# Performance work log

Measured on AMD Instinct MI355X. Metric: run time of the kernel, lower is better.

## Reference

```python
import jax, jax.numpy as jnp
import numpy as np
from jax import lax

B, C, H, W = 32, 3, 256, 256
P, D, E, K = 16, 256, 8, 2
HP, WP = H // P, W // P
N = HP * WP
GATE_IN = C * P * P  # 768
GATE_HID = D // 2    # 128


def _mk(key, shape, scale=0.02):
    return scale * jax.random.normal(key, shape, dtype=jnp.float32)


def setup_inputs() -> dict:
    key = jax.random.key(0)
    ks = jax.random.split(key, 20)
    inp = {
        "x": jax.random.normal(ks[0], (B, C, H, W), dtype=jnp.float32),
        # gate MLP: Linear(768,128) -> ReLU -> Linear(128,8)
        "g_w1": _mk(ks[1], (GATE_HID, GATE_IN)),
        "g_b1": jnp.zeros((GATE_HID,), jnp.float32),
        "g_w2": _mk(ks[2], (E, GATE_HID)),
        "g_b2": jnp.zeros((E,), jnp.float32),
        # per-expert CNN params, stacked with leading expert dim E
        "dw1_w": _mk(ks[3], (E, 3, 1, 3, 3)),   "dw1_b": jnp.zeros((E, 3), jnp.float32),
        "pw1_w": _mk(ks[4], (E, 64, 3, 1, 1)),  "pw1_b": jnp.zeros((E, 64), jnp.float32),
        "dw2_w": _mk(ks[5], (E, 64, 1, 3, 3)),  "dw2_b": jnp.zeros((E, 64), jnp.float32),
        "pw2_w": _mk(ks[6], (E, 128, 64, 1, 1)), "pw2_b": jnp.zeros((E, 128), jnp.float32),
        "dw3_w": _mk(ks[7], (E, 128, 1, 3, 3)), "dw3_b": jnp.zeros((E, 128), jnp.float32),
        "pw3_w": _mk(ks[8], (E, D, 128, 1, 1)), "pw3_b": jnp.zeros((E, D), jnp.float32),
    }
    return inp


def _dwconv(x, w, b, stride):
    # depthwise 3x3, padding 1; x: [n, c, h, w]; w: [c, 1, 3, 3]
    c = x.shape[1]
    y = lax.conv_general_dilated(
        x, w, (stride, stride), ((1, 1), (1, 1)),
        dimension_numbers=("NCHW", "OIHW", "NCHW"), feature_group_count=c)
    return jax.nn.relu(y + b[None, :, None, None])


def _pwconv(x, w, b):
    # pointwise 1x1 conv as GEMM; w: [o, c, 1, 1]
    y = jnp.einsum("nchw,oc->nohw", x, w[:, :, 0, 0]) + b[None, :, None, None]
    return jax.nn.relu(y)


def _expert(x, dw1w, dw1b, pw1w, pw1b, dw2w, dw2b, pw2w, pw2b, dw3w, dw3b, pw3w, pw3b):
    # x: [BN, 3, 16, 16] -> [BN, D]
    x = _pwconv(_dwconv(x, dw1w, dw1b, 2), pw1w, pw1b)   # [BN, 64, 8, 8]
    x = _pwconv(_dwconv(x, dw2w, dw2b, 2), pw2w, pw2b)   # [BN, 128, 4, 4]
    x = _pwconv(_dwconv(x, dw3w, dw3b, 2), pw3w, pw3b)   # [BN, 256, 2, 2]
    return x.mean(axis=(2, 3))                            # adaptive avg pool to 1x1


def reference(x, g_w1, g_b1, g_w2, g_b2,
              dw1_w, dw1_b, pw1_w, pw1_b, dw2_w, dw2_b, pw2_w, pw2_b,
              dw3_w, dw3_b, pw3_w, pw3_b):
    b = x.shape[0]
    # nn.Unfold(kernel=P, stride=P): columns ordered (c, di, dj)
    patches = x.reshape(b, C, HP, P, WP, P).transpose(0, 2, 4, 1, 3, 5)  # [B,hp,wp,C,P,P]
    patches_sp = patches.reshape(b * N, C, P, P)
    patches_flat = patches_sp.reshape(b * N, GATE_IN)

    # gate (eval mode: dropout is identity)
    h = jax.nn.relu(patches_flat @ g_w1.T + g_b1)
    logits = h @ g_w2.T + g_b2                       # [BN, E]
    topk_vals, topk_idx = lax.top_k(logits, K)       # [BN, K]
    weights = jax.nn.softmax(topk_vals, axis=-1)
    one_hot = jax.nn.one_hot(topk_idx, E, dtype=x.dtype)   # [BN, K, E]
    routing = (one_hot * weights[..., None]).sum(axis=1)   # [BN, E]

    # run all experts densely (as the original does), then combine
    expert_outs = jax.vmap(_expert, in_axes=(None,) + (0,) * 12)(
        patches_sp, dw1_w, dw1_b, pw1_w, pw1_b, dw2_w, dw2_b,
        pw2_w, pw2_b, dw3_w, dw3_b, pw3_w, pw3_b)   # [E, BN, D]
    out = jnp.einsum("ne,end->nd", routing, expert_outs)  # [BN, D]

    features = out.reshape(b, HP, WP, D).transpose(0, 3, 1, 2)  # [B, D, hp, wp]
    load_balance_loss = jnp.float32(0.0)  # eval mode
    return features, load_balance_loss
```

## Files before the change

kernel.cpp:

```cpp
#include <hip/hip_runtime.h>

#define BN 8192
#define GIN 768
#define SL 2560

#define O_ROUTE_I 0UL
#define O_ROUTE_W (O_ROUTE_I + (size_t)BN*2*4)
#define O_COUNTS  (O_ROUTE_W + (size_t)BN*2*4)
#define O_LISTS   (O_COUNTS + 256)
#define O_PW2T    (O_LISTS + (size_t)8*BN*4)
#define O_PW3T    (O_PW2T + (size_t)8*64*128*4)
#define O_SLOT    (O_PW3T + (size_t)8*128*256*4)

__global__ __launch_bounds__(256) void k0_prep(const float* __restrict__ pw2w,
                                               const float* __restrict__ pw3w,
                                               float* __restrict__ pw2t,
                                               float* __restrict__ pw3t,
                                               int* __restrict__ counts)
{
    int tid = blockIdx.x * 256 + threadIdx.x;
    if (tid < 8) counts[tid] = 0;
    for (int idx = tid; idx < 8 * 128 * 64; idx += 256 * 256) {
        int e = idx >> 13; int r = idx & 8191; int oc = r >> 6; int c = r & 63;
        pw2t[(size_t)e * 8192 + c * 128 + oc] = pw2w[idx];
    }
    for (int idx = tid; idx < 8 * 256 * 128; idx += 256 * 256) {
        int e = idx >> 15; int r = idx & 32767; int oc = r >> 7; int c = r & 127;
        pw3t[(size_t)e * 32768 + c * 256 + oc] = pw3w[idx];
    }
}

__global__ __launch_bounds__(256) void k1_gate(
    const float* __restrict__ x, const float* __restrict__ w1,
    const float* __restrict__ b1, const float* __restrict__ w2,
    const float* __restrict__ b2,
    int* __restrict__ route_i, float* __restrict__ route_w,
    int* __restrict__ counts, int* __restrict__ lists)
{
    __shared__ __align__(16) float A[32][20];
    __shared__ __align__(16) float Wl[32][132];
    __shared__ float hl[16][132];
    __shared__ float ll[16][8];

    int tid = threadIdx.x;
    int pblk = blockIdx.x * 16;

    int pgrp = tid & 7;
    int hgrp = tid >> 3;
    float acc[2][4] = {};

    int sp  = tid >> 4;
    int sk2 = (tid & 15) * 2;
    int swh = tid >> 1;
    int swk = (tid & 1) * 16;

    int patchA = pblk + sp;
    int bA = patchA >> 8; int nA = patchA & 255; int hpA = nA >> 4; int wpA = nA & 15;

    for (int kc = 0; kc < GIN; kc += 32) {
        {
            int k = kc + sk2;
            int c = k >> 8; int rem = k & 255; int ri = rem >> 4; int j = rem & 15;
            const float* src = x + (((size_t)(bA * 3 + c) * 256 + hpA * 16 + ri) * 256 + wpA * 16 + j);
            float2 a2 = *reinterpret_cast<const float2*>(src);
            A[sk2][sp] = a2.x; A[sk2 + 1][sp] = a2.y;
        }
        {
            const float* wsrc = w1 + (size_t)swh * GIN + kc + swk;
            #pragma unroll
            for (int qq = 0; qq < 4; qq++) {
                float4 w4 = *reinterpret_cast<const float4*>(wsrc + qq * 4);
                Wl[swk + qq * 4 + 0][swh] = w4.x; Wl[swk + qq * 4 + 1][swh] = w4.y;
                Wl[swk + qq * 4 + 2][swh] = w4.z; Wl[swk + qq * 4 + 3][swh] = w4.w;
            }
        }
        __syncthreads();
        float cacc[2][4] = {};
        #pragma unroll
        for (int k2 = 0; k2 < 32; k2++) {
            float2 av = *reinterpret_cast<const float2*>(&A[k2][pgrp * 2]);
            float4 wv = *reinterpret_cast<const float4*>(&Wl[k2][hgrp * 4]);
            float aa[2] = {av.x, av.y};
            float ww[4] = {wv.x, wv.y, wv.z, wv.w};
            #pragma unroll
            for (int i = 0; i < 2; i++) {
                #pragma unroll
                for (int jj = 0; jj < 4; jj++) cacc[i][jj] += aa[i] * ww[jj];
            }
        }
        #pragma unroll
        for (int i = 0; i < 2; i++) {
            #pragma unroll
            for (int jj = 0; jj < 4; jj++) acc[i][jj] += cacc[i][jj];
        }
        __syncthreads();
    }

    #pragma unroll
    for (int jj = 0; jj < 4; jj++) {
        float bb = b1[hgrp * 4 + jj];
        #pragma unroll
        for (int i = 0; i < 2; i++) {
            float v = acc[i][jj] + bb;
            hl[pgrp * 2 + i][hgrp * 4 + jj] = v > 0.f ? v : 0.f;
        }
    }
    __syncthreads();

    if (tid < 128) {
        int lp = tid >> 3; int le = tid & 7;
        float lacc = b2[le];
        const float* wrow = w2 + le * 128;
        for (int h = 0; h < 128; h++) lacc += hl[lp][h] * wrow[h];
        ll[lp][le] = lacc;
    }
    __syncthreads();

    if (tid < 16) {
        int patch = pblk + tid;
        float v[8];
        #pragma unroll
        for (int e = 0; e < 8; e++) v[e] = ll[tid][e];
        int e0 = 0; float m0 = v[0];
        #pragma unroll
        for (int e = 1; e < 8; e++) if (v[e] > m0) { m0 = v[e]; e0 = e; }
        int e1 = -1; float m1 = -3.0e38f;
        #pragma unroll
        for (int e = 0; e < 8; e++) if (e != e0 && v[e] > m1) { m1 = v[e]; e1 = e; }
        float t = expf(m1 - m0);
        float w0 = 1.f / (1.f + t);
        float w1v = t * w0;
        route_i[patch * 2] = e0; route_i[patch * 2 + 1] = e1;
        route_w[patch * 2] = w0; route_w[patch * 2 + 1] = w1v;
        int p0 = atomicAdd(&counts[e0], 1);
        lists[e0 * BN + p0] = patch * 2;
        int p1 = atomicAdd(&counts[e1], 1);
        lists[e1 * BN + p1] = patch * 2 + 1;
    }
}

__global__ __launch_bounds__(256, 4) void k23_expert(
    const float* __restrict__ x, const int* __restrict__ counts,
    const int* __restrict__ lists,
    const float* __restrict__ dw1w, const float* __restrict__ dw1b,
    const float* __restrict__ pw1w, const float* __restrict__ pw1b,
    const float* __restrict__ dw2w, const float* __restrict__ dw2b,
    const float* __restrict__ pw2t, const float* __restrict__ pw2b,
    const float* __restrict__ dw3w, const float* __restrict__ dw3b,
    const float* __restrict__ pw3t, const float* __restrict__ pw3b,
    float* __restrict__ slot)
{
    __shared__ __align__(16) float buf[4][SL];

    int e = blockIdx.x & 7;
    int chunk = blockIdx.x >> 3;
    int cnt = counts[e];
    int base = chunk * 4;
    if (base >= cnt) return;
    int n_en = cnt - base; if (n_en > 4) n_en = 4;
    int tid = threadIdx.x;
    int wid = tid >> 6;
    int l = tid & 63;
    int en_l = l >> 4;
    int q = l & 15;

    int myidx = base + wid; if (myidx >= cnt) myidx = cnt - 1;
    int pslot = lists[e * BN + myidx];
    int patch = pslot >> 1;
    int b = patch >> 8, nn = patch & 255, hp = nn >> 4, wp = nn & 15;

    float* pl  = buf[wid];
    float* d1  = buf[wid] + 2048;
    float* d2t = buf[wid];

    {
        int r = l >> 2; int j4 = (l & 3) * 4;
        #pragma unroll
        for (int c = 0; c < 3; c++) {
            const float* src = x + (((size_t)(b * 3 + c) * 256 + hp * 16 + r) * 256 + wp * 16 + j4);
            float4 v = *reinterpret_cast<const float4*>(src);
            *reinterpret_cast<float4*>(&pl[c * 320 + r * 20 + j4]) = v;
        }
    }

    {
        int oh = l >> 3, ow = l & 7;
        #pragma unroll
        for (int c = 0; c < 3; c++) {
            const float* w9 = dw1w + (e * 3 + c) * 9;
            float acc = dw1b[e * 3 + c];
            #pragma unroll
            for (int ki = 0; ki < 3; ki++) {
                int ih = oh * 2 - 1 + ki;
                if ((unsigned)ih < 16u) {
                    #pragma unroll
                    for (int kj = 0; kj < 3; kj++) {
                        int iw = ow * 2 - 1 + kj;
                        if ((unsigned)iw < 16u) acc += pl[c * 320 + ih * 20 + iw] * w9[ki * 3 + kj];
                    }
                }
            }
            d1[c * 64 + l] = acc > 0.f ? acc : 0.f;
        }
    }

    {
        const float* w3 = pw1w + (e * 64 + l) * 3;
        float pw0 = w3[0], pw1v = w3[1], pw2v = w3[2];
        float pb = pw1b[e * 64 + l];
        const float* w9 = dw2w + (e * 64 + l) * 9;
        float wd[9];
        #pragma unroll
        for (int i = 0; i < 9; i++) wd[i] = w9[i];
        float bd = dw2b[e * 64 + l];

        int dcol = (l + wid * 4) & 63;
        float rc[8] = {};
        float re[8], ro[8];

        #pragma unroll
        for (int oh = 0; oh < 4; oh++) {
            #pragma unroll
            for (int half = 0; half < 2; half++) {
                float* dst = half ? ro : re;
                const float* d1b = d1 + (oh * 2 + half) * 8;
                float4 x0 = *reinterpret_cast<const float4*>(&d1b[0]);
                float4 x1 = *reinterpret_cast<const float4*>(&d1b[4]);
                float4 y0 = *reinterpret_cast<const float4*>(&d1b[64]);
                float4 y1 = *reinterpret_cast<const float4*>(&d1b[68]);
                float4 z0 = *reinterpret_cast<const float4*>(&d1b[128]);
                float4 z1 = *reinterpret_cast<const float4*>(&d1b[132]);
                float v;
                v = pb + x0.x * pw0 + y0.x * pw1v + z0.x * pw2v; dst[0] = v > 0.f ? v : 0.f;
                v = pb + x0.y * pw0 + y0.y * pw1v + z0.y * pw2v; dst[1] = v > 0.f ? v : 0.f;
                v = pb + x0.z * pw0 + y0.z * pw1v + z0.z * pw2v; dst[2] = v > 0.f ? v : 0.f;
                v = pb + x0.w * pw0 + y0.w * pw1v + z0.w * pw2v; dst[3] = v > 0.f ? v : 0.f;
                v = pb + x1.x * pw0 + y1.x * pw1v + z1.x * pw2v; dst[4] = v > 0.f ? v : 0.f;
                v = pb + x1.y * pw0 + y1.y * pw1v + z1.y * pw2v; dst[5] = v > 0.f ? v : 0.f;
                v = pb + x1.z * pw0 + y1.z * pw1v + z1.z * pw2v; dst[6] = v > 0.f ? v : 0.f;
                v = pb + x1.w * pw0 + y1.w * pw1v + z1.w * pw2v; dst[7] = v > 0.f ? v : 0.f;
            }
            #pragma unroll
            for (int ow = 0; ow < 4; ow++) {
                float acc = bd;
                if (oh > 0) {
                    #pragma unroll
                    for (int kj = 0; kj < 3; kj++) {
                        int iw = ow * 2 - 1 + kj;
                        if ((unsigned)iw < 8u) acc += rc[iw] * wd[kj];
                    }
                }
                #pragma unroll
                for (int kj = 0; kj < 3; kj++) {
                    int iw = ow * 2 - 1 + kj;
                    if ((unsigned)iw < 8u) acc += re[iw] * wd[3 + kj];
                }
                #pragma unroll
                for (int kj = 0; kj < 3; kj++) {
                    int iw = ow * 2 - 1 + kj;
                    if ((unsigned)iw < 8u) acc += ro[iw] * wd[6 + kj];
                }
                d2t[(oh * 4 + ow) * 68 + dcol] = acc > 0.f ? acc : 0.f;
            }
            #pragma unroll
            for (int i = 0; i < 8; i++) rc[i] = ro[i];
        }
    }
    __syncthreads();

    {
        const float* dsl = buf[en_l];
        int ocg = q & 3, pq = q >> 2;
        int oc0 = wid * 32 + ocg * 8;
        int p0 = pq * 4;
        float acc[8][4] = {};
        const float* wbase = pw2t + (size_t)e * 8192;
        #pragma unroll 2
        for (int c4 = 0; c4 < 16; c4++) {
            int col = (c4 * 4 + en_l * 4) & 63;
            float4 a0 = *reinterpret_cast<const float4*>(&dsl[(p0 + 0) * 68 + col]);
            float4 a1 = *reinterpret_cast<const float4*>(&dsl[(p0 + 1) * 68 + col]);
            float4 a2 = *reinterpret_cast<const float4*>(&dsl[(p0 + 2) * 68 + col]);
            float4 a3 = *reinterpret_cast<const float4*>(&dsl[(p0 + 3) * 68 + col]);
            float av[4][4] = {{a0.x, a1.x, a2.x, a3.x}, {a0.y, a1.y, a2.y, a3.y},
                              {a0.z, a1.z, a2.z, a3.z}, {a0.w, a1.w, a2.w, a3.w}};
            #pragma unroll
            for (int cc = 0; cc < 4; cc++) {
                int c = c4 * 4 + cc;
                float4 wa = *reinterpret_cast<const float4*>(wbase + c * 128 + oc0);
                float4 wb = *reinterpret_cast<const float4*>(wbase + c * 128 + oc0 + 4);
                float wv[8] = {wa.x, wa.y, wa.z, wa.w, wb.x, wb.y, wb.z, wb.w};
                #pragma unroll
                for (int j = 0; j < 8; j++) {
                    #pragma unroll
                    for (int i = 0; i < 4; i++) acc[j][i] += wv[j] * av[cc][i];
                }
            }
        }
        __syncthreads();
        int g = oc0 >> 3;
        float* p2w = buf[en_l];
        #pragma unroll
        for (int j = 0; j < 8; j++) {
            float bb = pw2b[e * 128 + oc0 + j];
            #pragma unroll
            for (int i = 0; i < 4; i++) {
                float v = acc[j][i] + bb;
                p2w[(oc0 + j) * 16 + ((p0 + i + g + en_l) & 15)] = v > 0.f ? v : 0.f;
            }
        }
    }
    __syncthreads();

    {
        float* p2 = buf[wid];
        float* d3 = buf[wid] + 2048;
        #pragma unroll
        for (int chb = 0; chb < 128; chb += 64) {
            int ch = chb + l;
            int grp = ch >> 3;
            const float* w9 = dw3w + (e * 128 + ch) * 9;
            float bb = dw3b[e * 128 + ch];
            #pragma unroll
            for (int pos = 0; pos < 4; pos++) {
                int oh = pos >> 1, ow = pos & 1;
                float acc = bb;
                #pragma unroll
                for (int ki = 0; ki < 3; ki++) {
                    int ih = oh * 2 - 1 + ki;
                    if ((unsigned)ih < 4u) {
                        #pragma unroll
                        for (int kj = 0; kj < 3; kj++) {
                            int iw = ow * 2 - 1 + kj;
                            if ((unsigned)iw < 4u)
                                acc += p2[ch * 16 + ((ih * 4 + iw + grp + wid) & 15)] * w9[ki * 3 + kj];
                        }
                    }
                }
                d3[((ch + wid * 4) & 127) * 4 + pos] = acc > 0.f ? acc : 0.f;
            }
        }
    }
    __syncthreads();

    {
        int oc0 = wid * 64 + q * 4;
        const float* d3b = buf[en_l] + 2048;
        const float* wbase = pw3t + (size_t)e * 32768;
        float acc[4][4] = {};
        #pragma unroll 4
        for (int c = 0; c < 128; c++) {
            float4 a = *reinterpret_cast<const float4*>(&d3b[((c + en_l * 4) & 127) * 4]);
            float4 w = *reinterpret_cast<const float4*>(wbase + c * 256 + oc0);
            float av[4] = {a.x, a.y, a.z, a.w};
            float wv[4] = {w.x, w.y, w.z, w.w};
            #pragma unroll
            for (int j = 0; j < 4; j++) {
                #pragma unroll
                for (int i = 0; i < 4; i++) acc[j][i] += wv[j] * av[i];
            }
        }
        if (en_l < n_en) {
            int ps_f = lists[e * BN + base + en_l];
            float o4[4];
            #pragma unroll
            for (int j = 0; j < 4; j++) {
                float bb = pw3b[e * 256 + oc0 + j];
                float s = 0.f;
                #pragma unroll
                for (int i = 0; i < 4; i++) {
                    float v = acc[j][i] + bb;
                    s += (v > 0.f ? v : 0.f);
                }
                o4[j] = 0.25f * s;
            }
            *reinterpret_cast<float4*>(slot + (size_t)ps_f * 256 + oc0) =
                make_float4(o4[0], o4[1], o4[2], o4[3]);
        }
    }
}

__global__ __launch_bounds__(256) void k4_comb(
    const float* __restrict__ slot, const float* __restrict__ route_w,
    float* __restrict__ out)
{
    __shared__ float cl[16][257];
    int bx = blockIdx.x;
    int b = bx >> 4; int hp = bx & 15;
    int tid = threadIdx.x;
    int d = tid;
    for (int wp = 0; wp < 16; wp++) {
        int n = (b * 16 + hp) * 16 + wp;
        float w0 = route_w[n * 2], w1 = route_w[n * 2 + 1];
        float v = w0 * slot[(size_t)(n * 2) * 256 + d] + w1 * slot[(size_t)(n * 2 + 1) * 256 + d];
        cl[wp][d] = v;
    }
    __syncthreads();
    int wp = tid & 15; int dg = tid >> 4;
    for (int r = 0; r < 16; r++) {
        int dd = r * 16 + dg;
        out[(((size_t)b * 256 + dd) * 16 + hp) * 16 + wp] = cl[wp][dd];
    }
    if (bx == 0 && tid == 0) out[(size_t)BN * 256] = 0.0f;
}

extern "C" void kernel_launch(void* const* d_in, const int* in_sizes, int n_in,
                              void* d_out, int out_size, void* d_ws, size_t ws_size,
                              hipStream_t stream)
{
    const float* x    = (const float*)d_in[0];
    const float* gw1  = (const float*)d_in[1];
    const float* gb1  = (const float*)d_in[2];
    const float* gw2  = (const float*)d_in[3];
    const float* gb2  = (const float*)d_in[4];
    const float* dw1w = (const float*)d_in[5];
    const float* dw1b = (const float*)d_in[6];
    const float* pw1w = (const float*)d_in[7];
    const float* pw1b = (const float*)d_in[8];
    const float* dw2w = (const float*)d_in[9];
    const float* dw2b = (const float*)d_in[10];
    const float* pw2w = (const float*)d_in[11];
    const float* pw2b = (const float*)d_in[12];
    const float* dw3w = (const float*)d_in[13];
    const float* dw3b = (const float*)d_in[14];
    const float* pw3w = (const float*)d_in[15];
    const float* pw3b = (const float*)d_in[16];

    char* ws = (char*)d_ws;
    int*   route_i = (int*)(ws + O_ROUTE_I);
    float* route_w = (float*)(ws + O_ROUTE_W);
    int*   counts  = (int*)(ws + O_COUNTS);
    int*   lists   = (int*)(ws + O_LISTS);
    float* pw2t    = (float*)(ws + O_PW2T);
    float* pw3t    = (float*)(ws + O_PW3T);
    float* slot    = (float*)(ws + O_SLOT);
    float* out     = (float*)d_out;

    hipLaunchKernelGGL(k0_prep, dim3(256), dim3(256), 0, stream,
                       pw2w, pw3w, pw2t, pw3t, counts);
    hipLaunchKernelGGL(k1_gate, dim3(BN / 16), dim3(256), 0, stream,
                       x, gw1, gb1, gw2, gb2, route_i, route_w, counts, lists);
    hipLaunchKernelGGL(k23_expert, dim3(8 * 2048), dim3(256), 0, stream,
                       x, counts, lists, dw1w, dw1b, pw1w, pw1b, dw2w, dw2b,
                       pw2t, pw2b, dw3w, dw3b, pw3t, pw3b, slot);
    hipLaunchKernelGGL(k4_comb, dim3(512), dim3(256), 0, stream,
                       slot, route_w, out);
}
```

Before: 520.2 us.

## Double expert kernel block to 512 threads, splitting each patch's stages across two waves

The expert kernel now launches 512 threads per block, with two wavefronts per patch instead of one. The dw2 rows, the dw3 channels and the pw2/pw3 output channels are split between the two waves, which halves per-thread accumulators and work. A new barrier is added after the dw1 stage, and that stage is done by only half the waves. The aim is more parallelism and latency hiding per block at the cost of extra synchronisation, some duplicated pw1 row computation, and idle waves during dw1.

```diff
diff --git a/kernel.cpp b/kernel.cpp
--- a/kernel.cpp
+++ b/kernel.cpp
@@ -139,7 +139,58 @@
     }
 }
 
-__global__ __launch_bounds__(256, 4) void k23_expert(
+__device__ __forceinline__ void pw1_row(const float* __restrict__ d1, int row,
+                                        float pb, float pw0, float pw1v, float pw2v,
+                                        float* __restrict__ dst)
+{
+    const float* d1b = d1 + row * 8;
+    float4 x0 = *reinterpret_cast<const float4*>(&d1b[0]);
+    float4 x1 = *reinterpret_cast<const float4*>(&d1b[4]);
+    float4 y0 = *reinterpret_cast<const float4*>(&d1b[64]);
+    float4 y1 = *reinterpret_cast<const float4*>(&d1b[68]);
+    float4 z0 = *reinterpret_cast<const float4*>(&d1b[128]);
+    float4 z1 = *reinterpret_cast<const float4*>(&d1b[132]);
+    float v;
+    v = pb + x0.x * pw0 + y0.x * pw1v + z0.x * pw2v; dst[0] = v > 0.f ? v : 0.f;
+    v = pb + x0.y * pw0 + y0.y * pw1v + z0.y * pw2v; dst[1] = v > 0.f ? v : 0.f;
+    v = pb + x0.z * pw0 + y0.z * pw1v + z0.z * pw2v; dst[2] = v > 0.f ? v : 0.f;
+    v = pb + x0.w * pw0 + y0.w * pw1v + z0.w * pw2v; dst[3] = v > 0.f ? v : 0.f;
+    v = pb + x1.x * pw0 + y1.x * pw1v + z1.x * pw2v; dst[4] = v > 0.f ? v : 0.f;
+    v = pb + x1.y * pw0 + y1.y * pw1v + z1.y * pw2v; dst[5] = v > 0.f ? v : 0.f;
+    v = pb + x1.z * pw0 + y1.z * pw1v + z1.z * pw2v; dst[6] = v > 0.f ? v : 0.f;
+    v = pb + x1.w * pw0 + y1.w * pw1v + z1.w * pw2v; dst[7] = v > 0.f ? v : 0.f;
+}
+
+__device__ __forceinline__ void dw2_row(int oh, bool use_rc,
+                                        const float* rc, const float* re, const float* ro,
+                                        const float* wd, float bd,
+                                        float* __restrict__ d2t, int dcol)
+{
+    #pragma unroll
+    for (int ow = 0; ow < 4; ow++) {
+        float acc = bd;
+        if (use_rc) {
+            #pragma unroll
+            for (int kj = 0; kj < 3; kj++) {
+                int iw = ow * 2 - 1 + kj;
+                if ((unsigned)iw < 8u) acc += rc[iw] * wd[kj];
+            }
+        }
+        #pragma unroll
+        for (int kj = 0; kj < 3; kj++) {
+            int iw = ow * 2 - 1 + kj;
+            if ((unsigned)iw < 8u) acc += re[iw] * wd[3 + kj];
+        }
+        #pragma unroll
+        for (int kj = 0; kj < 3; kj++) {
+            int iw = ow * 2 - 1 + kj;
+            if ((unsigned)iw < 8u) acc += ro[iw] * wd[6 + kj];
+        }
+        d2t[(oh * 4 + ow) * 68 + dcol] = acc > 0.f ? acc : 0.f;
+    }
+}
+
+__global__ __launch_bounds__(512, 8) void k23_expert(
     const float* __restrict__ x, const int* __restrict__ counts,
     const int* __restrict__ lists,
     const float* __restrict__ dw1w, const float* __restrict__ dw1b,
@@ -161,48 +212,52 @@
     int tid = threadIdx.x;
     int wid = tid >> 6;
     int l = tid & 63;
+    int en_p = wid & 3;
+    int half = wid >> 2;
     int en_l = l >> 4;
     int q = l & 15;
 
-    int myidx = base + wid; if (myidx >= cnt) myidx = cnt - 1;
+    int myidx = base + en_p; if (myidx >= cnt) myidx = cnt - 1;
     int pslot = lists[e * BN + myidx];
     int patch = pslot >> 1;
     int b = patch >> 8, nn = patch & 255, hp = nn >> 4, wp = nn & 15;
 
-    float* pl  = buf[wid];
-    float* d1  = buf[wid] + 2048;
-    float* d2t = buf[wid];
-
-    {
-        int r = l >> 2; int j4 = (l & 3) * 4;
-        #pragma unroll
-        for (int c = 0; c < 3; c++) {
-            const float* src = x + (((size_t)(b * 3 + c) * 256 + hp * 16 + r) * 256 + wp * 16 + j4);
-            float4 v = *reinterpret_cast<const float4*>(src);
-            *reinterpret_cast<float4*>(&pl[c * 320 + r * 20 + j4]) = v;
-        }
-    }
-
-    {
-        int oh = l >> 3, ow = l & 7;
-        #pragma unroll
-        for (int c = 0; c < 3; c++) {
-            const float* w9 = dw1w + (e * 3 + c) * 9;
-            float acc = dw1b[e * 3 + c];
-            #pragma unroll
-            for (int ki = 0; ki < 3; ki++) {
-                int ih = oh * 2 - 1 + ki;
-                if ((unsigned)ih < 16u) {
-                    #pragma unroll
-                    for (int kj = 0; kj < 3; kj++) {
-                        int iw = ow * 2 - 1 + kj;
-                        if ((unsigned)iw < 16u) acc += pl[c * 320 + ih * 20 + iw] * w9[ki * 3 + kj];
+    float* pl  = buf[en_p];
+    float* d1  = buf[en_p] + 2048;
+    float* d2t = buf[en_p];
+
+    if (half == 0) {
+        {
+            int r = l >> 2; int j4 = (l & 3) * 4;
+            #pragma unroll
+            for (int c = 0; c < 3; c++) {
+                const float* src = x + (((size_t)(b * 3 + c) * 256 + hp * 16 + r) * 256 + wp * 16 + j4);
+                float4 v = *reinterpret_cast<const float4*>(src);
+                *reinterpret_cast<float4*>(&pl[c * 320 + r * 20 + j4]) = v;
+            }
+        }
+        {
+            int oh = l >> 3, ow = l & 7;
+            #pragma unroll
+            for (int c = 0; c < 3; c++) {
+                const float* w9 = dw1w + (e * 3 + c) * 9;
+                float acc = dw1b[e * 3 + c];
+                #pragma unroll
+                for (int ki = 0; ki < 3; ki++) {
+                    int ih = oh * 2 - 1 + ki;
+                    if ((unsigned)ih < 16u) {
+                        #pragma unroll
+                        for (int kj = 0; kj < 3; kj++) {
+                            int iw = ow * 2 - 1 + kj;
+                            if ((unsigned)iw < 16u) acc += pl[c * 320 + ih * 20 + iw] * w9[ki * 3 + kj];
+                        }
                     }
                 }
-            }
-            d1[c * 64 + l] = acc > 0.f ? acc : 0.f;
-        }
-    }
+                d1[c * 64 + l] = acc > 0.f ? acc : 0.f;
+            }
+        }
+    }
+    __syncthreads();
 
     {
         const float* w3 = pw1w + (e * 64 + l) * 3;
@@ -213,57 +268,28 @@
         #pragma unroll
         for (int i = 0; i < 9; i++) wd[i] = w9[i];
         float bd = dw2b[e * 64 + l];
-
-        int dcol = (l + wid * 4) & 63;
-        float rc[8] = {};
-        float re[8], ro[8];
-
-        #pragma unroll
-        for (int oh = 0; oh < 4; oh++) {
-            #pragma unroll
-            for (int half = 0; half < 2; half++) {
-                float* dst = half ? ro : re;
-                const float* d1b = d1 + (oh * 2 + half) * 8;
-                float4 x0 = *reinterpret_cast<const float4*>(&d1b[0]);
-                float4 x1 = *reinterpret_cast<const float4*>(&d1b[4]);
-                float4 y0 = *reinterpret_cast<const float4*>(&d1b[64]);
-                float4 y1 = *reinterpret_cast<const float4*>(&d1b[68]);
-                float4 z0 = *reinterpret_cast<const float4*>(&d1b[128]);
-                float4 z1 = *reinterpret_cast<const float4*>(&d1b[132]);
-                float v;
-                v = pb + x0.x * pw0 + y0.x * pw1v + z0.x * pw2v; dst[0] = v > 0.f ? v : 0.f;
-                v = pb + x0.y * pw0 + y0.y * pw1v + z0.y * pw2v; dst[1] = v > 0.f ? v : 0.f;
-                v = pb + x0.z * pw0 + y0.z * pw1v + z0.z * pw2v; dst[2] = v > 0.f ? v : 0.f;
-                v = pb + x0.w * pw0 + y0.w * pw1v + z0.w * pw2v; dst[3] = v > 0.f ? v : 0.f;
-                v = pb + x1.x * pw0 + y1.x * pw1v + z1.x * pw2v; dst[4] = v > 0.f ? v : 0.f;
-                v = pb + x1.y * pw0 + y1.y * pw1v + z1.y * pw2v; dst[5] = v > 0.f ? v : 0.f;
-                v = pb + x1.z * pw0 + y1.z * pw1v + z1.z * pw2v; dst[6] = v > 0.f ? v : 0.f;
-                v = pb + x1.w * pw0 + y1.w * pw1v + z1.w * pw2v; dst[7] = v > 0.f ? v : 0.f;
-            }
-            #pragma unroll
-            for (int ow = 0; ow < 4; ow++) {
-                float acc = bd;
-                if (oh > 0) {
-                    #pragma unroll
-                    for (int kj = 0; kj < 3; kj++) {
-                        int iw = ow * 2 - 1 + kj;
-                        if ((unsigned)iw < 8u) acc += rc[iw] * wd[kj];
-                    }
-                }
-                #pragma unroll
-                for (int kj = 0; kj < 3; kj++) {
-                    int iw = ow * 2 - 1 + kj;
-                    if ((unsigned)iw < 8u) acc += re[iw] * wd[3 + kj];
-                }
-                #pragma unroll
-                for (int kj = 0; kj < 3; kj++) {
-                    int iw = ow * 2 - 1 + kj;
-                    if ((unsigned)iw < 8u) acc += ro[iw] * wd[6 + kj];
-                }
-                d2t[(oh * 4 + ow) * 68 + dcol] = acc > 0.f ? acc : 0.f;
-            }
+        int dcol = (l + en_p * 4) & 63;
+
+        float rc[8], re[8], ro[8];
+        if (half == 0) {
+            pw1_row(d1, 0, pb, pw0, pw1v, pw2v, re);
+            pw1_row(d1, 1, pb, pw0, pw1v, pw2v, ro);
+            dw2_row(0, false, rc, re, ro, wd, bd, d2t, dcol);
             #pragma unroll
             for (int i = 0; i < 8; i++) rc[i] = ro[i];
+            pw1_row(d1, 2, pb, pw0, pw1v, pw2v, re);
+            pw1_row(d1, 3, pb, pw0, pw1v, pw2v, ro);
+            dw2_row(1, true, rc, re, ro, wd, bd, d2t, dcol);
+        } else {
+            pw1_row(d1, 3, pb, pw0, pw1v, pw2v, rc);
+            pw1_row(d1, 4, pb, pw0, pw1v, pw2v, re);
+            pw1_row(d1, 5, pb, pw0, pw1v, pw2v, ro);
+            dw2_row(2, true, rc, re, ro, wd, bd, d2t, dcol);
+            #pragma unroll
+            for (int i = 0; i < 8; i++) rc[i] = ro[i];
+            pw1_row(d1, 6, pb, pw0, pw1v, pw2v, re);
+            pw1_row(d1, 7, pb, pw0, pw1v, pw2v, ro);
+            dw2_row(3, true, rc, re, ro, wd, bd, d2t, dcol);
         }
     }
     __syncthreads();
@@ -271,9 +297,9 @@
     {
         const float* dsl = buf[en_l];
         int ocg = q & 3, pq = q >> 2;
-        int oc0 = wid * 32 + ocg * 8;
+        int oc0 = wid * 16 + ocg * 4;
         int p0 = pq * 4;
-        float acc[8][4] = {};
+        float acc[4][4] = {};
         const float* wbase = pw2t + (size_t)e * 8192;
         #pragma unroll 2
         for (int c4 = 0; c4 < 16; c4++) {
@@ -287,11 +313,10 @@
             #pragma unroll
             for (int cc = 0; cc < 4; cc++) {
                 int c = c4 * 4 + cc;
-                float4 wa = *reinterpret_cast<const float4*>(wbase + c * 128 + oc0);
-                float4 wb = *reinterpret_cast<const float4*>(wbase + c * 128 + oc0 + 4);
-                float wv[8] = {wa.x, wa.y, wa.z, wa.w, wb.x, wb.y, wb.z, wb.w};
+                float4 w = *reinterpret_cast<const float4*>(wbase + c * 128 + oc0);
+                float wv[4] = {w.x, w.y, w.z, w.w};
                 #pragma unroll
-                for (int j = 0; j < 8; j++) {
+                for (int j = 0; j < 4; j++) {
                     #pragma unroll
                     for (int i = 0; i < 4; i++) acc[j][i] += wv[j] * av[cc][i];
                 }
@@ -299,72 +324,68 @@
         }
         __syncthreads();
         int g = oc0 >> 3;
-        float* p2w = buf[en_l];
-        #pragma unroll
-        for (int j = 0; j < 8; j++) {
+        float* p2w_ = buf[en_l];
+        #pragma unroll
+        for (int j = 0; j < 4; j++) {
             float bb = pw2b[e * 128 + oc0 + j];
             #pragma unroll
             for (int i = 0; i < 4; i++) {
                 float v = acc[j][i] + bb;
-                p2w[(oc0 + j) * 16 + ((p0 + i + g + en_l) & 15)] = v > 0.f ? v : 0.f;
+                p2w_[(oc0 + j) * 16 + ((p0 + i + g + en_l) & 15)] = v > 0.f ? v : 0.f;
             }
         }
     }
     __syncthreads();
 
     {
-        float* p2 = buf[wid];
-        float* d3 = buf[wid] + 2048;
-        #pragma unroll
-        for (int chb = 0; chb < 128; chb += 64) {
-            int ch = chb + l;
-            int grp = ch >> 3;
-            const float* w9 = dw3w + (e * 128 + ch) * 9;
-            float bb = dw3b[e * 128 + ch];
-            #pragma unroll
-            for (int pos = 0; pos < 4; pos++) {
-                int oh = pos >> 1, ow = pos & 1;
-                float acc = bb;
-                #pragma unroll
-                for (int ki = 0; ki < 3; ki++) {
-                    int ih = oh * 2 - 1 + ki;
-                    if ((unsigned)ih < 4u) {
-                        #pragma unroll
-                        for (int kj = 0; kj < 3; kj++) {
-                            int iw = ow * 2 - 1 + kj;
-                            if ((unsigned)iw < 4u)
-                                acc += p2[ch * 16 + ((ih * 4 + iw + grp + wid) & 15)] * w9[ki * 3 + kj];
-                        }
+        float* p2 = buf[en_p];
+        float* d3 = buf[en_p] + 2048;
+        int ch = half * 64 + l;
+        int grp = ch >> 3;
+        const float* w9 = dw3w + (e * 128 + ch) * 9;
+        float bb = dw3b[e * 128 + ch];
+        #pragma unroll
+        for (int pos = 0; pos < 4; pos++) {
+            int oh = pos >> 1, ow = pos & 1;
+            float acc = bb;
+            #pragma unroll
+            for (int ki = 0; ki < 3; ki++) {
+                int ih = oh * 2 - 1 + ki;
+                if ((unsigned)ih < 4u) {
+                    #pragma unroll
+                    for (int kj = 0; kj < 3; kj++) {
+                        int iw = ow * 2 - 1 + kj;
+                        if ((unsigned)iw < 4u)
+                            acc += p2[ch * 16 + ((ih * 4 + iw + grp + en_p) & 15)] * w9[ki * 3 + kj];
                     }
                 }
-                d3[((ch + wid * 4) & 127) * 4 + pos] = acc > 0.f ? acc : 0.f;
-            }
+            }
+            d3[((ch + en_p * 4) & 127) * 4 + pos] = acc > 0.f ? acc : 0.f;
         }
     }
     __syncthreads();
 
     {
-        int oc0 = wid * 64 + q * 4;
+        int oc0 = wid * 32 + q * 2;
         const float* d3b = buf[en_l] + 2048;
         const float* wbase = pw3t + (size_t)e * 32768;
-        float acc[4][4] = {};
+        float acc[2][4] = {};
         #pragma unroll 4
         for (int c = 0; c < 128; c++) {
             float4 a = *reinterpret_cast<const float4*>(&d3b[((c + en_l * 4) & 127) * 4]);
-            float4 w = *reinterpret_cast<const float4*>(wbase + c * 256 + oc0);
+            float2 w = *reinterpret_cast<const float2*>(wbase + c * 256 + oc0);
             float av[4] = {a.x, a.y, a.z, a.w};
-            float wv[4] = {w.x, w.y, w.z, w.w};
-            #pragma unroll
-            for (int j = 0; j < 4; j++) {
-                #pragma unroll
-                for (int i = 0; i < 4; i++) acc[j][i] += wv[j] * av[i];
+            #pragma unroll
+            for (int i = 0; i < 4; i++) {
+                acc[0][i] += w.x * av[i];
+                acc[1][i] += w.y * av[i];
             }
         }
         if (en_l < n_en) {
             int ps_f = lists[e * BN + base + en_l];
-            float o4[4];
-            #pragma unroll
-            for (int j = 0; j < 4; j++) {
+            float o2[2];
+            #pragma unroll
+            for (int j = 0; j < 2; j++) {
                 float bb = pw3b[e * 256 + oc0 + j];
                 float s = 0.f;
                 #pragma unroll
@@ -372,10 +393,10 @@
                     float v = acc[j][i] + bb;
                     s += (v > 0.f ? v : 0.f);
                 }
-                o4[j] = 0.25f * s;
-            }
-            *reinterpret_cast<float4*>(slot + (size_t)ps_f * 256 + oc0) =
-                make_float4(o4[0], o4[1], o4[2], o4[3]);
+                o2[j] = 0.25f * s;
+            }
+            *reinterpret_cast<float2*>(slot + (size_t)ps_f * 256 + oc0) =
+                make_float2(o2[0], o2[1]);
         }
     }
 }
@@ -440,7 +461,7 @@
                        pw2w, pw3w, pw2t, pw3t, counts);
     hipLaunchKernelGGL(k1_gate, dim3(BN / 16), dim3(256), 0, stream,
                        x, gw1, gb1, gw2, gb2, route_i, route_w, counts, lists);
-    hipLaunchKernelGGL(k23_expert, dim3(8 * 2048), dim3(256), 0, stream,
+    hipLaunchKernelGGL(k23_expert, dim3(8 * 2048), dim3(512), 0, stream,
                        x, counts, lists, dw1w, dw1b, pw1w, pw1b, dw2w, dw2b,
                        pw2t, pw2b, dw3w, dw3b, pw3t, pw3b, slot);
     hipLaunchKernelGGL(k4_comb, dim3(512), dim3(256), 0, stream,
```

New measurement: 718.6 us. 1.38x slower.

## Make each wavefront own one patch end-to-end and drop block syncs

Applied to the files above, without the earlier changes.

Restructures the expert kernel so each 64-lane wavefront processes a single patch through all stages. The pw2 GEMM, dw3 and pw3 stages now run per-wave with per-thread channel ownership, so the pw2 output stays in registers and feeds dw3 directly. This removes all __syncthreads and the cross-wave sharing of activations, and shrinks shared memory per wave. The trade-off is that weight loads from global memory are no longer amortised across four patches, and per-thread register pressure rises (32 accumulators plus the dw3 temporaries).

```diff
diff --git a/kernel.cpp b/kernel.cpp
--- a/kernel.cpp
+++ b/kernel.cpp
@@ -2,7 +2,7 @@
 
 #define BN 8192
 #define GIN 768
-#define SL 2560
+#define SL 1664
 
 #define O_ROUTE_I 0UL
 #define O_ROUTE_W (O_ROUTE_I + (size_t)BN*2*4)
@@ -139,6 +139,28 @@
     }
 }
 
+__device__ __forceinline__ void pw1_row(const float* __restrict__ d1, int row,
+                                        float pb, float pw0, float pw1v, float pw2v,
+                                        float* __restrict__ dst)
+{
+    const float* d1b = d1 + row * 8;
+    float4 x0 = *reinterpret_cast<const float4*>(&d1b[0]);
+    float4 x1 = *reinterpret_cast<const float4*>(&d1b[4]);
+    float4 y0 = *reinterpret_cast<const float4*>(&d1b[64]);
+    float4 y1 = *reinterpret_cast<const float4*>(&d1b[68]);
+    float4 z0 = *reinterpret_cast<const float4*>(&d1b[128]);
+    float4 z1 = *reinterpret_cast<const float4*>(&d1b[132]);
+    float v;
+    v = pb + x0.x * pw0 + y0.x * pw1v + z0.x * pw2v; dst[0] = v > 0.f ? v : 0.f;
+    v = pb + x0.y * pw0 + y0.y * pw1v + z0.y * pw2v; dst[1] = v > 0.f ? v : 0.f;
+    v = pb + x0.z * pw0 + y0.z * pw1v + z0.z * pw2v; dst[2] = v > 0.f ? v : 0.f;
+    v = pb + x0.w * pw0 + y0.w * pw1v + z0.w * pw2v; dst[3] = v > 0.f ? v : 0.f;
+    v = pb + x1.x * pw0 + y1.x * pw1v + z1.x * pw2v; dst[4] = v > 0.f ? v : 0.f;
+    v = pb + x1.y * pw0 + y1.y * pw1v + z1.y * pw2v; dst[5] = v > 0.f ? v : 0.f;
+    v = pb + x1.z * pw0 + y1.z * pw1v + z1.z * pw2v; dst[6] = v > 0.f ? v : 0.f;
+    v = pb + x1.w * pw0 + y1.w * pw1v + z1.w * pw2v; dst[7] = v > 0.f ? v : 0.f;
+}
+
 __global__ __launch_bounds__(256, 4) void k23_expert(
     const float* __restrict__ x, const int* __restrict__ counts,
     const int* __restrict__ lists,
@@ -157,21 +179,17 @@
     int cnt = counts[e];
     int base = chunk * 4;
     if (base >= cnt) return;
-    int n_en = cnt - base; if (n_en > 4) n_en = 4;
     int tid = threadIdx.x;
-    int wid = tid >> 6;
-    int l = tid & 63;
-    int en_l = l >> 4;
-    int q = l & 15;
-
-    int myidx = base + wid; if (myidx >= cnt) myidx = cnt - 1;
-    int pslot = lists[e * BN + myidx];
+    int en = tid >> 6; int l = tid & 63;
+    if (base + en >= cnt) return;
+    int pslot = lists[e * BN + base + en];
     int patch = pslot >> 1;
     int b = patch >> 8, nn = patch & 255, hp = nn >> 4, wp = nn & 15;
 
-    float* pl  = buf[wid];
-    float* d1  = buf[wid] + 2048;
-    float* d2t = buf[wid];
+    float* pl  = buf[en];
+    float* d1  = buf[en] + 1152;
+    float* d2t = buf[en];
+    float* d3  = buf[en] + 1152;
 
     {
         int r = l >> 2; int j4 = (l & 3) * 4;
@@ -214,32 +232,13 @@
         for (int i = 0; i < 9; i++) wd[i] = w9[i];
         float bd = dw2b[e * 64 + l];
 
-        int dcol = (l + wid * 4) & 63;
         float rc[8] = {};
         float re[8], ro[8];
 
         #pragma unroll
         for (int oh = 0; oh < 4; oh++) {
-            #pragma unroll
-            for (int half = 0; half < 2; half++) {
-                float* dst = half ? ro : re;
-                const float* d1b = d1 + (oh * 2 + half) * 8;
-                float4 x0 = *reinterpret_cast<const float4*>(&d1b[0]);
-                float4 x1 = *reinterpret_cast<const float4*>(&d1b[4]);
-                float4 y0 = *reinterpret_cast<const float4*>(&d1b[64]);
-                float4 y1 = *reinterpret_cast<const float4*>(&d1b[68]);
-                float4 z0 = *reinterpret_cast<const float4*>(&d1b[128]);
-                float4 z1 = *reinterpret_cast<const float4*>(&d1b[132]);
-                float v;
-                v = pb + x0.x * pw0 + y0.x * pw1v + z0.x * pw2v; dst[0] = v > 0.f ? v : 0.f;
-                v = pb + x0.y * pw0 + y0.y * pw1v + z0.y * pw2v; dst[1] = v > 0.f ? v : 0.f;
-                v = pb + x0.z * pw0 + y0.z * pw1v + z0.z * pw2v; dst[2] = v > 0.f ? v : 0.f;
-                v = pb + x0.w * pw0 + y0.w * pw1v + z0.w * pw2v; dst[3] = v > 0.f ? v : 0.f;
-                v = pb + x1.x * pw0 + y1.x * pw1v + z1.x * pw2v; dst[4] = v > 0.f ? v : 0.f;
-                v = pb + x1.y * pw0 + y1.y * pw1v + z1.y * pw2v; dst[5] = v > 0.f ? v : 0.f;
-                v = pb + x1.z * pw0 + y1.z * pw1v + z1.z * pw2v; dst[6] = v > 0.f ? v : 0.f;
-                v = pb + x1.w * pw0 + y1.w * pw1v + z1.w * pw2v; dst[7] = v > 0.f ? v : 0.f;
-            }
+            pw1_row(d1, oh * 2 + 0, pb, pw0, pw1v, pw2v, re);
+            pw1_row(d1, oh * 2 + 1, pb, pw0, pw1v, pw2v, ro);
             #pragma unroll
             for (int ow = 0; ow < 4; ow++) {
                 float acc = bd;
@@ -260,71 +259,49 @@
                     int iw = ow * 2 - 1 + kj;
                     if ((unsigned)iw < 8u) acc += ro[iw] * wd[6 + kj];
                 }
-                d2t[(oh * 4 + ow) * 68 + dcol] = acc > 0.f ? acc : 0.f;
+                d2t[l * 18 + oh * 4 + ow] = acc > 0.f ? acc : 0.f;
             }
             #pragma unroll
             for (int i = 0; i < 8; i++) rc[i] = ro[i];
         }
     }
-    __syncthreads();
 
     {
-        const float* dsl = buf[en_l];
-        int ocg = q & 3, pq = q >> 2;
-        int oc0 = wid * 32 + ocg * 8;
-        int p0 = pq * 4;
-        float acc[8][4] = {};
+        int ch0 = 2 * l;
         const float* wbase = pw2t + (size_t)e * 8192;
-        #pragma unroll 2
-        for (int c4 = 0; c4 < 16; c4++) {
-            int col = (c4 * 4 + en_l * 4) & 63;
-            float4 a0 = *reinterpret_cast<const float4*>(&dsl[(p0 + 0) * 68 + col]);
-            float4 a1 = *reinterpret_cast<const float4*>(&dsl[(p0 + 1) * 68 + col]);
-            float4 a2 = *reinterpret_cast<const float4*>(&dsl[(p0 + 2) * 68 + col]);
-            float4 a3 = *reinterpret_cast<const float4*>(&dsl[(p0 + 3) * 68 + col]);
-            float av[4][4] = {{a0.x, a1.x, a2.x, a3.x}, {a0.y, a1.y, a2.y, a3.y},
-                              {a0.z, a1.z, a2.z, a3.z}, {a0.w, a1.w, a2.w, a3.w}};
-            #pragma unroll
-            for (int cc = 0; cc < 4; cc++) {
-                int c = c4 * 4 + cc;
-                float4 wa = *reinterpret_cast<const float4*>(wbase + c * 128 + oc0);
-                float4 wb = *reinterpret_cast<const float4*>(wbase + c * 128 + oc0 + 4);
-                float wv[8] = {wa.x, wa.y, wa.z, wa.w, wb.x, wb.y, wb.z, wb.w};
-                #pragma unroll
-                for (int j = 0; j < 8; j++) {
-                    #pragma unroll
-                    for (int i = 0; i < 4; i++) acc[j][i] += wv[j] * av[cc][i];
-                }
-            }
-        }
-        __syncthreads();
-        int g = oc0 >> 3;
-        float* p2w = buf[en_l];
-        #pragma unroll
-        for (int j = 0; j < 8; j++) {
-            float bb = pw2b[e * 128 + oc0 + j];
-            #pragma unroll
-            for (int i = 0; i < 4; i++) {
-                float v = acc[j][i] + bb;
-                p2w[(oc0 + j) * 16 + ((p0 + i + g + en_l) & 15)] = v > 0.f ? v : 0.f;
-            }
-        }
-    }
-    __syncthreads();
-
-    {
-        float* p2 = buf[wid];
-        float* d3 = buf[wid] + 2048;
-        #pragma unroll
-        for (int chb = 0; chb < 128; chb += 64) {
-            int ch = chb + l;
-            int grp = ch >> 3;
-            const float* w9 = dw3w + (e * 128 + ch) * 9;
-            float bb = dw3b[e * 128 + ch];
+        float a0[16] = {}, a1[16] = {};
+        #pragma unroll 4
+        for (int c = 0; c < 64; c++) {
+            float2 w = *reinterpret_cast<const float2*>(wbase + c * 128 + ch0);
+            const float* dr = d2t + c * 18;
+            #pragma unroll
+            for (int j = 0; j < 8; j++) {
+                float2 av = *reinterpret_cast<const float2*>(dr + 2 * j);
+                a0[2 * j]     += w.x * av.x;
+                a0[2 * j + 1] += w.x * av.y;
+                a1[2 * j]     += w.y * av.x;
+                a1[2 * j + 1] += w.y * av.y;
+            }
+        }
+        {
+            float b0 = pw2b[e * 128 + ch0];
+            float b1v = pw2b[e * 128 + ch0 + 1];
+            #pragma unroll
+            for (int p = 0; p < 16; p++) {
+                float v0 = a0[p] + b0;  a0[p] = v0 > 0.f ? v0 : 0.f;
+                float v1 = a1[p] + b1v; a1[p] = v1 > 0.f ? v1 : 0.f;
+            }
+        }
+        {
+            const float* w90 = dw3w + (e * 128 + ch0) * 9;
+            const float* w91 = w90 + 9;
+            float bb0 = dw3b[e * 128 + ch0];
+            float bb1 = dw3b[e * 128 + ch0 + 1];
+            float o0[4], o1[4];
             #pragma unroll
             for (int pos = 0; pos < 4; pos++) {
                 int oh = pos >> 1, ow = pos & 1;
-                float acc = bb;
+                float s0 = bb0, s1 = bb1;
                 #pragma unroll
                 for (int ki = 0; ki < 3; ki++) {
                     int ih = oh * 2 - 1 + ki;
@@ -332,25 +309,28 @@
                         #pragma unroll
                         for (int kj = 0; kj < 3; kj++) {
                             int iw = ow * 2 - 1 + kj;
-                            if ((unsigned)iw < 4u)
-                                acc += p2[ch * 16 + ((ih * 4 + iw + grp + wid) & 15)] * w9[ki * 3 + kj];
+                            if ((unsigned)iw < 4u) {
+                                s0 += a0[ih * 4 + iw] * w90[ki * 3 + kj];
+                                s1 += a1[ih * 4 + iw] * w91[ki * 3 + kj];
+                            }
                         }
                     }
                 }
-                d3[((ch + wid * 4) & 127) * 4 + pos] = acc > 0.f ? acc : 0.f;
-            }
-        }
-    }
-    __syncthreads();
+                o0[pos] = s0 > 0.f ? s0 : 0.f;
+                o1[pos] = s1 > 0.f ? s1 : 0.f;
+            }
+            *reinterpret_cast<float4*>(&d3[ch0 * 4])     = make_float4(o0[0], o0[1], o0[2], o0[3]);
+            *reinterpret_cast<float4*>(&d3[ch0 * 4 + 4]) = make_float4(o1[0], o1[1], o1[2], o1[3]);
+        }
+    }
 
     {
-        int oc0 = wid * 64 + q * 4;
-        const float* d3b = buf[en_l] + 2048;
+        int oc0 = l * 4;
         const float* wbase = pw3t + (size_t)e * 32768;
         float acc[4][4] = {};
         #pragma unroll 4
         for (int c = 0; c < 128; c++) {
-            float4 a = *reinterpret_cast<const float4*>(&d3b[((c + en_l * 4) & 127) * 4]);
+            float4 a = *reinterpret_cast<const float4*>(&d3[c * 4]);
             float4 w = *reinterpret_cast<const float4*>(wbase + c * 256 + oc0);
             float av[4] = {a.x, a.y, a.z, a.w};
             float wv[4] = {w.x, w.y, w.z, w.w};
@@ -360,23 +340,20 @@
                 for (int i = 0; i < 4; i++) acc[j][i] += wv[j] * av[i];
             }
         }
-        if (en_l < n_en) {
-            int ps_f = lists[e * BN + base + en_l];
-            float o4[4];
-            #pragma unroll
-            for (int j = 0; j < 4; j++) {
-                float bb = pw3b[e * 256 + oc0 + j];
-                float s = 0.f;
-                #pragma unroll
-                for (int i = 0; i < 4; i++) {
-                    float v = acc[j][i] + bb;
-                    s += (v > 0.f ? v : 0.f);
-                }
-                o4[j] = 0.25f * s;
-            }
-            *reinterpret_cast<float4*>(slot + (size_t)ps_f * 256 + oc0) =
-                make_float4(o4[0], o4[1], o4[2], o4[3]);
-        }
+        float o4[4];
+        #pragma unroll
+        for (int j = 0; j < 4; j++) {
+            float bb = pw3b[e * 256 + oc0 + j];
+            float s = 0.f;
+            #pragma unroll
+            for (int i = 0; i < 4; i++) {
+                float v = acc[j][i] + bb;
+                s += (v > 0.f ? v : 0.f);
+            }
+            o4[j] = 0.25f * s;
+        }
+        *reinterpret_cast<float4*>(slot + (size_t)pslot * 256 + oc0) =
+            make_float4(o4[0], o4[1], o4[2], o4[3]);
     }
 }
 
```

New measurement: 488.8 us. 1.06x faster.
